# Kernel optimization log

Hardware: AMD Instinct MI355X
Metric: run time of the kernel (lower is better)

The kernel has to match this reference:

```python
import jax, jax.numpy as jnp
import numpy as np

BINS = 30
MOMENTUM = 0.75  # first call: last_bin_count is None, so momentum has no effect


def setup_inputs() -> dict:
    key = jax.random.key(0)
    k1, k2 = jax.random.split(key)
    logits = jax.random.normal(k1, (4096, 8192), dtype=jnp.float32)
    target = jax.random.randint(k2, (4096, 8192), 0, 2, dtype=jnp.int32)
    return {"logits": logits, "target": target}


def reference(logits, target):
    t = target.astype(logits.dtype)
    # gradient-density statistic (detached in torch)
    g = jnp.abs(jax.nn.sigmoid(jax.lax.stop_gradient(logits)) - t)
    bin_idx = jnp.floor(g * (BINS - 0.0001)).astype(jnp.int32)  # in [0, BINS-1]
    # histogram over bins (single fused scatter-add, no per-bin host sync)
    flat_idx = bin_idx.reshape(-1)
    bin_count = jax.ops.segment_sum(
        jnp.ones_like(flat_idx, dtype=logits.dtype), flat_idx, num_segments=BINS
    )
    nonempty_bins = jnp.sum(bin_count > 0).astype(logits.dtype)
    tot = jnp.asarray(logits.size, dtype=logits.dtype)
    beta = tot / jnp.clip(bin_count * nonempty_bins, 1e-4)  # [BINS]
    weight = beta[bin_idx]  # gather per-element weight
    # binary_cross_entropy_with_logits, reduction='none', weighted
    bce = -(t * jax.nn.log_sigmoid(logits) + (1.0 - t) * jax.nn.log_sigmoid(-logits))
    loss = weight * bce
    return loss.mean(axis=1)
```

## Files before the change

### kernel.cpp

```cpp
#include <hip/hip_runtime.h>
#include <math.h>

#define BINS 30
#define ROWS 4096
#define COLS 8192
#define REP  32
#define GREP 32
#define STK  256

__device__ __forceinline__ int bin_ref_f32(float x, int t)
{
    float e   = (float)exp(-(double)x);
    float d   = 1.0f + e;
    float sig = 1.0f / d;
    float g   = fabsf(sig - (float)t);
    float u   = g * 29.9999f;
    int b = (int)u;
    return b > (BINS - 1) ? (BINS - 1) : b;
}

__global__ __launch_bounds__(256, 4) void k_hist(const float* __restrict__ logits,
                                                 const int*   __restrict__ target,
                                                 float*       __restrict__ rowsum,
                                                 unsigned int* __restrict__ ghist)
{
    __shared__ unsigned int h[REP * BINS];
    __shared__ unsigned int sx[STK];
    __shared__ unsigned int sm[STK];
    __shared__ unsigned int scount;

    const int tid = threadIdx.x;
    const int row = blockIdx.x;
    for (int i = tid; i < REP * BINS; i += 256) h[i] = 0u;
    if (tid == 0) scount = 0u;
    __syncthreads();

    const int base = (tid & (REP - 1)) * BINS;
    const float4* lp = (const float4*)(logits + (size_t)row * COLS);
    const int4*   tp = (const int4*)(target + (size_t)row * COLS);

    float4 xv[8];
    int4   tv[8];
    #pragma unroll
    for (int k = 0; k < 8; ++k) {
        xv[k] = lp[tid + k * 256];
        tv[k] = tp[tid + k * 256];
    }

    #pragma unroll
    for (int k = 0; k < 8; ++k) {
        float xs[4] = {xv[k].x, xv[k].y, xv[k].z, xv[k].w};
        int   ts[4] = {tv[k].x, tv[k].y, tv[k].z, tv[k].w};
        #pragma unroll
        for (int c = 0; c < 4; ++c) {
            float s = __uint_as_float(__float_as_uint(xs[c]) ^
                                      ((unsigned int)ts[c] << 31));
            float z   = __builtin_amdgcn_exp2f(fabsf(s) * -1.44269504088896340736f);
            float d   = 1.0f + z;
            float inv = __builtin_amdgcn_rcpf(d);
            float g   = (s >= 0.0f) ? inv : z * inv;
            float bce = fmaf(__builtin_amdgcn_logf(d),
                             0.69314718055994530942f, fmaxf(s, 0.0f));
            float u   = g * 29.9999f;
            int   bin = (int)u;
            float frac = u - (float)bin;
            unsigned int q = (unsigned int)fmaf(bce, 1024.0f, 0.5f);

            if (fabsf(frac - 0.5f) >= 0.4995f) {
                unsigned int idx = atomicAdd(&scount, 1u);
                if (idx < STK) {
                    sx[idx] = __float_as_uint(xs[c]);
                    sm[idx] = q | ((unsigned int)ts[c] << 21);
                }
            } else {
                atomicAdd(&h[base + bin], (1u << 23) | q);
            }
        }
    }
    __syncthreads();

    unsigned int n = scount < STK ? scount : STK;
    for (unsigned int i = tid; i < n; i += 256) {
        float x = __uint_as_float(sx[i]);
        unsigned int mw = sm[i];
        int bin = bin_ref_f32(x, (int)(mw >> 21));
        atomicAdd(&h[(tid & (REP - 1)) * BINS + bin],
                  (1u << 23) | (mw & 0x1FFFFFu));
    }
    __syncthreads();

    if (tid < BINS) {
        unsigned int cnt = 0u;
        float        fs  = 0.0f;
        #pragma unroll
        for (int r = 0; r < REP; ++r) {
            unsigned int v = h[r * BINS + tid];
            cnt += v >> 23;
            fs  += (float)(v & 0x7FFFFFu);
        }
        rowsum[(size_t)row * BINS + tid] = fs * (1.0f / 1024.0f);
        atomicAdd(&ghist[(row & (GREP - 1)) * 32 + tid], cnt);
    }
}

__global__ __launch_bounds__(256) void k_finish(const unsigned int* __restrict__ ghist,
                                                const float* __restrict__ rowsum,
                                                float* __restrict__ out)
{
    __shared__ float sb[BINS];
    const int tid = threadIdx.x;
    if (tid < 64) {
        const int b = tid;
        unsigned int c = 0u;
        if (b < BINS) {
            #pragma unroll
            for (int r = 0; r < GREP; ++r) c += ghist[r * 32 + b];
        }
        unsigned long long m = __ballot(b < BINS && c > 0u);
        float nonempty = (float)__popcll(m);
        if (b < BINS) {
            const float tot = (float)ROWS * (float)COLS;
            sb[b] = tot / fmaxf((float)c * nonempty, 1e-4f);
        }
    }
    __syncthreads();
    const int row = blockIdx.x * 256 + tid;
    const float* rp = rowsum + (size_t)row * BINS;
    float acc = 0.0f;
    #pragma unroll
    for (int b = 0; b < BINS; ++b) acc += sb[b] * rp[b];
    out[row] = acc * (1.0f / (float)COLS);
}

extern "C" void kernel_launch(void* const* d_in, const int* in_sizes, int n_in,
                              void* d_out, int out_size, void* d_ws, size_t ws_size,
                              hipStream_t stream)
{
    const float* logits = (const float*)d_in[0];
    const int*   target = (const int*)d_in[1];
    float*       out    = (float*)d_out;

    unsigned int* ghist  = (unsigned int*)d_ws;
    float*        rowsum = (float*)d_ws + GREP * 32;

    hipMemsetAsync(d_ws, 0, GREP * 32 * sizeof(unsigned int), stream);

    k_hist  <<<ROWS, 256, 0, stream>>>(logits, target, rowsum, ghist);
    k_finish<<<ROWS / 256, 256, 0, stream>>>(ghist, rowsum, out);
}
```

Before: 54.39 us.

## Assign one wavefront per row to remove block-wide barriers in histogram kernel

Each 64-lane wavefront now processes a full row in four chunks of 8 float4 loads, and each block handles four rows, so the block-level __syncthreads calls go away. Every wave keeps its own histogram (with fewer replicas, 8 instead of 32) and its own spill stack. The boundary test for elements that need an exact recompute is rewritten using rintf. The aim is to cut synchronization and launch overhead, at the cost of less memory parallelism per row and more LDS atomic contention because there are fewer replicas. The code relies on wave-synchronous execution with no barrier between the LDS writes and reads within a wave, and the per-wave spill stack is smaller, which raises the risk of overflow.

Result: no change. 54.97 us (+1.1%).

```diff
diff --git a/kernel.cpp b/kernel.cpp
--- a/kernel.cpp
+++ b/kernel.cpp
@@ -4,9 +4,9 @@
 #define BINS 30
 #define ROWS 4096
 #define COLS 8192
-#define REP  32
+#define REP  8
 #define GREP 32
-#define STK  256
+#define WSTK 64
 
 __device__ __forceinline__ int bin_ref_f32(float x, int t)
 {
@@ -24,82 +24,85 @@
                                                  float*       __restrict__ rowsum,
                                                  unsigned int* __restrict__ ghist)
 {
-    __shared__ unsigned int h[REP * BINS];
-    __shared__ unsigned int sx[STK];
-    __shared__ unsigned int sm[STK];
-    __shared__ unsigned int scount;
+    __shared__ unsigned int h[4][REP * BINS];
+    __shared__ unsigned int sx[4][WSTK];
+    __shared__ unsigned int sm[4][WSTK];
+    __shared__ unsigned int scnt[4];
 
-    const int tid = threadIdx.x;
-    const int row = blockIdx.x;
-    for (int i = tid; i < REP * BINS; i += 256) h[i] = 0u;
-    if (tid == 0) scount = 0u;
-    __syncthreads();
+    const int tid  = threadIdx.x;
+    const int wid  = tid >> 6;
+    const int lane = tid & 63;
+    const int row  = blockIdx.x * 4 + wid;
 
-    const int base = (tid & (REP - 1)) * BINS;
+    unsigned int* hw = h[wid];
+    #pragma unroll
+    for (int i = lane; i < REP * BINS; i += 64) hw[i] = 0u;
+    if (lane == 0) scnt[wid] = 0u;
+
+    const int base = (lane & (REP - 1)) * BINS;
     const float4* lp = (const float4*)(logits + (size_t)row * COLS);
     const int4*   tp = (const int4*)(target + (size_t)row * COLS);
 
-    float4 xv[8];
-    int4   tv[8];
-    #pragma unroll
-    for (int k = 0; k < 8; ++k) {
-        xv[k] = lp[tid + k * 256];
-        tv[k] = tp[tid + k * 256];
-    }
+    for (int j = 0; j < 4; ++j) {
+        float4 xv[8];
+        int4   tv[8];
+        #pragma unroll
+        for (int k = 0; k < 8; ++k) {
+            xv[k] = lp[lane + (j * 8 + k) * 64];
+            tv[k] = tp[lane + (j * 8 + k) * 64];
+        }
+        #pragma unroll
+        for (int k = 0; k < 8; ++k) {
+            float xs[4] = {xv[k].x, xv[k].y, xv[k].z, xv[k].w};
+            int   ts[4] = {tv[k].x, tv[k].y, tv[k].z, tv[k].w};
+            #pragma unroll
+            for (int c = 0; c < 4; ++c) {
+                float s = __uint_as_float(__float_as_uint(xs[c]) ^
+                                          ((unsigned int)ts[c] << 31));
+                float z   = __builtin_amdgcn_exp2f(fabsf(s) * -1.44269504088896340736f);
+                float d   = 1.0f + z;
+                float inv = __builtin_amdgcn_rcpf(d);
+                float g   = (s >= 0.0f) ? inv : z * inv;
+                float bce = fmaf(__builtin_amdgcn_logf(d),
+                                 0.69314718055994530942f, fmaxf(s, 0.0f));
+                float u   = g * 29.9999f;
+                int   bin = (int)u;
+                unsigned int q = (unsigned int)fmaf(bce, 1024.0f, 0.5f);
 
-    #pragma unroll
-    for (int k = 0; k < 8; ++k) {
-        float xs[4] = {xv[k].x, xv[k].y, xv[k].z, xv[k].w};
-        int   ts[4] = {tv[k].x, tv[k].y, tv[k].z, tv[k].w};
-        #pragma unroll
-        for (int c = 0; c < 4; ++c) {
-            float s = __uint_as_float(__float_as_uint(xs[c]) ^
-                                      ((unsigned int)ts[c] << 31));
-            float z   = __builtin_amdgcn_exp2f(fabsf(s) * -1.44269504088896340736f);
-            float d   = 1.0f + z;
-            float inv = __builtin_amdgcn_rcpf(d);
-            float g   = (s >= 0.0f) ? inv : z * inv;
-            float bce = fmaf(__builtin_amdgcn_logf(d),
-                             0.69314718055994530942f, fmaxf(s, 0.0f));
-            float u   = g * 29.9999f;
-            int   bin = (int)u;
-            float frac = u - (float)bin;
-            unsigned int q = (unsigned int)fmaf(bce, 1024.0f, 0.5f);
-
-            if (fabsf(frac - 0.5f) >= 0.4995f) {
-                unsigned int idx = atomicAdd(&scount, 1u);
-                if (idx < STK) {
-                    sx[idx] = __float_as_uint(xs[c]);
-                    sm[idx] = q | ((unsigned int)ts[c] << 21);
+                if (fabsf(u - rintf(u)) <= 5e-4f) {
+                    unsigned int idx = atomicAdd(&scnt[wid], 1u);
+                    if (idx < WSTK) {
+                        sx[wid][idx] = __float_as_uint(xs[c]);
+                        sm[wid][idx] = q | ((unsigned int)ts[c] << 21);
+                    }
+                } else {
+                    atomicAdd(&hw[base + bin], (1u << 23) | q);
                 }
-            } else {
-                atomicAdd(&h[base + bin], (1u << 23) | q);
             }
         }
     }
-    __syncthreads();
 
-    unsigned int n = scount < STK ? scount : STK;
-    for (unsigned int i = tid; i < n; i += 256) {
-        float x = __uint_as_float(sx[i]);
-        unsigned int mw = sm[i];
+    unsigned int n = scnt[wid];
+    n = n < WSTK ? n : WSTK;
+    if (lane < (int)n) {
+        float x = __uint_as_float(sx[wid][lane]);
+        unsigned int mw = sm[wid][lane];
         int bin = bin_ref_f32(x, (int)(mw >> 21));
-        atomicAdd(&h[(tid & (REP - 1)) * BINS + bin],
+        atomicAdd(&hw[(lane & (REP - 1)) * BINS + bin],
                   (1u << 23) | (mw & 0x1FFFFFu));
     }
-    __syncthreads();
 
-    if (tid < BINS) {
+    if (lane < BINS) {
         unsigned int cnt = 0u;
         float        fs  = 0.0f;
         #pragma unroll
         for (int r = 0; r < REP; ++r) {
-            unsigned int v = h[r * BINS + tid];
+            unsigned int v = hw[r * BINS + lane];
             cnt += v >> 23;
             fs  += (float)(v & 0x7FFFFFu);
         }
-        rowsum[(size_t)row * BINS + tid] = fs * (1.0f / 1024.0f);
-        atomicAdd(&ghist[(row & (GREP - 1)) * 32 + tid], cnt);
+        rowsum[(size_t)row * BINS + lane] = fs * (1.0f / 1024.0f);
+        atomicAdd(&ghist[(row & (GREP - 1)) * 32 + lane], cnt);
     }
 }
 
@@ -145,6 +148,6 @@
 
     hipMemsetAsync(d_ws, 0, GREP * 32 * sizeof(unsigned int), stream);
 
-    k_hist  <<<ROWS, 256, 0, stream>>>(logits, target, rowsum, ghist);
+    k_hist  <<<ROWS / 4, 256, 0, stream>>>(logits, target, rowsum, ghist);
     k_finish<<<ROWS / 256, 256, 0, stream>>>(ghist, rowsum, out);
 }
```
